# Performance work log

Hardware: AMD Instinct MI355X
Metric: run time of the kernel (lower is better)

Reference implementation:

```python
import jax, jax.numpy as jnp
import numpy as np

B, S, H = 2, 2048, 1024
NUM_HEADS = 16
HEAD_DIM = H // NUM_HEADS  # 64
SCALE = HEAD_DIM ** -0.5


def apply_rope(x, cos, sin):
    # x: [B, nh, S, hd]; cos/sin: [1, 1, S, hd//2]
    x1 = x[..., ::2]
    x2 = x[..., 1::2]
    rotated = jnp.stack([x1 * cos - x2 * sin, x1 * sin + x2 * cos], axis=-1)
    return rotated.reshape(x.shape)


def setup_inputs() -> dict:
    key = jax.random.key(0)
    ks = jax.random.split(key, 7)
    return {
        "x": jax.random.normal(ks[0], (B, S, H), dtype=jnp.float32),
        "cos": jax.random.normal(ks[1], (S, HEAD_DIM // 2), dtype=jnp.float32),
        "sin": jax.random.normal(ks[2], (S, HEAD_DIM // 2), dtype=jnp.float32),
        "wq": jax.random.normal(ks[3], (H, H), dtype=jnp.float32) * (H ** -0.5),
        "wk": jax.random.normal(ks[4], (H, H), dtype=jnp.float32) * (H ** -0.5),
        "wv": jax.random.normal(ks[5], (H, H), dtype=jnp.float32) * (H ** -0.5),
        "wo": jax.random.normal(ks[6], (H, H), dtype=jnp.float32) * (H ** -0.5),
    }


def reference(x, cos, sin, wq, wk, wv, wo):
    b, s, h = x.shape
    nh, hd = NUM_HEADS, HEAD_DIM
    # torch Linear: y = x @ W.T
    q = (x @ wq.T).reshape(b, s, nh, hd).transpose(0, 2, 1, 3)  # [b, nh, s, hd]
    k = (x @ wk.T).reshape(b, s, nh, hd).transpose(0, 2, 1, 3)
    v = (x @ wv.T).reshape(b, s, nh, hd).transpose(0, 2, 1, 3)

    c = cos[None, None]  # [1,1,s,hd//2]
    sn = sin[None, None]
    q = apply_rope(q, c, sn)
    k = apply_rope(k, c, sn)

    scores = jnp.einsum("bhqd,bhkd->bhqk", q, k) * SCALE  # [b, nh, s, s]
    causal_mask = jnp.triu(jnp.ones((s, s), dtype=bool), k=1)
    scores = jnp.where(causal_mask[None, None], -jnp.inf, scores)
    attn = jax.nn.softmax(scores, axis=-1)
    out = jnp.einsum("bhqk,bhkd->bhqd", attn, v)  # [b, nh, s, hd]
    out = out.transpose(0, 2, 1, 3).reshape(b, s, h)
    return out @ wo.T
```

## Files before the change

### kernel.cpp

```cpp
#include <hip/hip_runtime.h>

typedef __attribute__((ext_vector_type(8))) __bf16 bf16x8;
typedef __attribute__((ext_vector_type(4))) float f32x4;
typedef __attribute__((ext_vector_type(4))) unsigned short ushort4v;

__device__ __forceinline__ unsigned short f2bf(float x) {
  union { float f; unsigned u; } v; v.f = x;
  unsigned r = v.u + 0x7fffu + ((v.u >> 16) & 1u);
  return (unsigned short)(r >> 16);
}

#define GLDS16(g, l) __builtin_amdgcn_global_load_lds( \
    (__attribute__((address_space(1))) void*)(g), \
    (__attribute__((address_space(3))) void*)(l), 16, 0, 0)

__global__ void cvt_f32_bf16(const float* __restrict__ src,
                             unsigned short* __restrict__ dst, int n4) {
  int i = blockIdx.x * blockDim.x + threadIdx.x;
  if (i >= n4) return;
  float4 v = reinterpret_cast<const float4*>(src)[i];
  ushort4v o;
  o.x = f2bf(v.x); o.y = f2bf(v.y); o.z = f2bf(v.z); o.w = f2bf(v.w);
  reinterpret_cast<ushort4v*>(dst)[i] = o;
}

template <int MODE>
__global__ __launch_bounds__(256) void gemm_bt(
    const unsigned short* __restrict__ A, const unsigned short* __restrict__ Bw,
    const float* __restrict__ cosT, const float* __restrict__ sinT,
    unsigned short* __restrict__ Qh, unsigned short* __restrict__ Kh,
    unsigned short* __restrict__ Vt, float* __restrict__ outF) {
  __shared__ __align__(16) unsigned char smA[2][8192];
  __shared__ __align__(16) unsigned char smB[2][8192];
  const int t = threadIdx.x;
  const int lane = t & 63, wvi = t >> 6;
  const int wr = wvi >> 1, wc = wvi & 1;
  const int g = lane >> 4, li = lane & 15;
  const int row0 = blockIdx.y * 128, col0 = blockIdx.x * 128;

  const int schunk = (t & 3) ^ ((t >> 2) & 3);
  const size_t arow = (size_t)(row0 + (t >> 2)) * 1024 + schunk * 8;
  const size_t brow = (size_t)(col0 + (t >> 2)) * 1024 + schunk * 8;

  f32x4 acc[4][4];
#pragma unroll
  for (int mi = 0; mi < 4; ++mi)
#pragma unroll
    for (int ni = 0; ni < 4; ++ni) acc[mi][ni] = (f32x4){0.f, 0.f, 0.f, 0.f};

  auto stage = [&](int buf, int k0) {
    GLDS16(A + arow + k0, &smA[buf][t * 16]);
    GLDS16(A + arow + 64 * 1024 + k0, &smA[buf][4096 + t * 16]);
    GLDS16(Bw + brow + k0, &smB[buf][t * 16]);
    GLDS16(Bw + brow + 64 * 1024 + k0, &smB[buf][4096 + t * 16]);
  };

  stage(0, 0);
  for (int kk = 0; kk < 32; ++kk) {
    __syncthreads();
    const int buf = kk & 1;
    if (kk < 31) stage(buf ^ 1, (kk + 1) * 32);
    bf16x8 af[4], bfr[4];
#pragma unroll
    for (int mi = 0; mi < 4; ++mi)
      af[mi] = *reinterpret_cast<const bf16x8*>(
          &smA[buf][((wr * 64 + mi * 16 + li) << 6) + ((g ^ (li & 3)) << 4)]);
#pragma unroll
    for (int ni = 0; ni < 4; ++ni)
      bfr[ni] = *reinterpret_cast<const bf16x8*>(
          &smB[buf][((wc * 64 + ni * 16 + li) << 6) + ((g ^ (li & 3)) << 4)]);
#pragma unroll
    for (int mi = 0; mi < 4; ++mi)
#pragma unroll
      for (int ni = 0; ni < 4; ++ni)
        acc[mi][ni] = __builtin_amdgcn_mfma_f32_16x16x32_bf16(
            af[mi], bfr[ni], acc[mi][ni], 0, 0, 0);
  }

#pragma unroll
  for (int mi = 0; mi < 4; ++mi) {
    const int rowb = row0 + wr * 64 + mi * 16 + g * 4;
#pragma unroll
    for (int ni = 0; ni < 4; ++ni) {
      const int col = col0 + wc * 64 + ni * 16 + li;
#pragma unroll
      for (int r = 0; r < 4; ++r) {
        float v = acc[mi][ni][r];
        const int rr = rowb + r;
        if (MODE == 1) {
          outF[(size_t)rr * 1024 + col] = v;
        } else {
          const int s = rr & 2047, b = rr >> 11;
          const int jj = col & 1023;
          const int h = jj >> 6, d = jj & 63;
          const int bh = b * 16 + h;
          const int typ = col >> 10;
          if (typ == 2) {
            Vt[((size_t)bh * 64 + d) * 2048 + s] = f2bf(v);
          } else {
            const float cs = cosT[s * 32 + (d >> 1)];
            const float sn = sinT[s * 32 + (d >> 1)];
            const float pr = __shfl_xor(v, 1);
            float rv = (d & 1) ? (pr * sn + v * cs) : (v * cs - pr * sn);
            if (typ == 0) rv *= 0.125f;
            unsigned short* dst = (typ == 0) ? Qh : Kh;
            dst[((size_t)bh * 2048 + s) * 64 + d] = f2bf(rv);
          }
        }
      }
    }
  }
}

__global__ __launch_bounds__(256) void attn_fwd(
    const unsigned short* __restrict__ Qh, const unsigned short* __restrict__ Kh,
    const unsigned short* __restrict__ Vt, unsigned short* __restrict__ Ob) {
  __shared__ __align__(16) unsigned char smK[2][8192];
  __shared__ __align__(16) unsigned char smV[2][8192];
  __shared__ __align__(16) unsigned short Plds[4][16][72];

  const int t = threadIdx.x, lane = t & 63, w = t >> 6;
  const int g = lane >> 4, li = lane & 15;
  const int qt = blockIdx.x, bh = blockIdx.y;
  const int q0 = qt * 64;

  bf16x8 qa[2];
  {
    const unsigned short* qrow =
        Qh + ((size_t)bh * 2048 + q0 + w * 16 + li) * 64 + g * 8;
    qa[0] = *reinterpret_cast<const bf16x8*>(qrow);
    qa[1] = *reinterpret_cast<const bf16x8*>(qrow + 32);
  }

  float m_[4], l_[4];
  f32x4 oacc[4];
#pragma unroll
  for (int r = 0; r < 4; ++r) { m_[r] = -1e30f; l_[r] = 0.f; }
#pragma unroll
  for (int dt = 0; dt < 4; ++dt) oacc[dt] = (f32x4){0.f, 0.f, 0.f, 0.f};

  const int ntile = qt + 1;

  auto stage = [&](int buf, int kt) {
    const int kv0 = kt * 64;
#pragma unroll
    for (int i = 0; i < 2; ++i) {
      const int e = i * 256 + t;
      const int row = e >> 3;
      const int sc = (e & 7) ^ (row & 7);
      GLDS16(Kh + ((size_t)bh * 2048 + kv0 + row) * 64 + sc * 8, &smK[buf][e * 16]);
      GLDS16(Vt + ((size_t)bh * 64 + row) * 2048 + kv0 + sc * 8, &smV[buf][e * 16]);
    }
  };

  stage(0, 0);
  for (int kt = 0; kt < ntile; ++kt) {
    __syncthreads();
    const int buf = kt & 1;
    if (kt + 1 < ntile) stage(buf ^ 1, kt + 1);

    f32x4 sacc[4];
#pragma unroll
    for (int ct = 0; ct < 4; ++ct) {
      const int rb = (ct * 16 + li) << 7;
      bf16x8 kb0 = *reinterpret_cast<const bf16x8*>(
          &smK[buf][rb + (((0 * 4 + g) ^ (li & 7)) << 4)]);
      bf16x8 kb1 = *reinterpret_cast<const bf16x8*>(
          &smK[buf][rb + (((1 * 4 + g) ^ (li & 7)) << 4)]);
      f32x4 z = (f32x4){0.f, 0.f, 0.f, 0.f};
      z = __builtin_amdgcn_mfma_f32_16x16x32_bf16(qa[0], kb0, z, 0, 0, 0);
      z = __builtin_amdgcn_mfma_f32_16x16x32_bf16(qa[1], kb1, z, 0, 0, 0);
      sacc[ct] = z;
    }
    if (kt == qt) {
#pragma unroll
      for (int ct = 0; ct < 4; ++ct)
#pragma unroll
        for (int r = 0; r < 4; ++r)
          if (ct * 16 + li > w * 16 + g * 4 + r) sacc[ct][r] = -1e30f;
    }
    float mnew[4], alpha[4], psum[4];
#pragma unroll
    for (int r = 0; r < 4; ++r) {
      float tm = fmaxf(fmaxf(sacc[0][r], sacc[1][r]), fmaxf(sacc[2][r], sacc[3][r]));
      tm = fmaxf(tm, __shfl_xor(tm, 1));
      tm = fmaxf(tm, __shfl_xor(tm, 2));
      tm = fmaxf(tm, __shfl_xor(tm, 4));
      tm = fmaxf(tm, __shfl_xor(tm, 8));
      const float mn = fmaxf(m_[r], tm);
      mnew[r] = mn;
      alpha[r] = __expf(m_[r] - mn);
      m_[r] = mn;
      psum[r] = 0.f;
    }
#pragma unroll
    for (int ct = 0; ct < 4; ++ct)
#pragma unroll
      for (int r = 0; r < 4; ++r) {
        const float p = __expf(sacc[ct][r] - mnew[r]);
        psum[r] += p;
        Plds[w][g * 4 + r][ct * 16 + li] = f2bf(p);
      }
#pragma unroll
    for (int r = 0; r < 4; ++r) {
      float ps = psum[r];
      ps += __shfl_xor(ps, 1);
      ps += __shfl_xor(ps, 2);
      ps += __shfl_xor(ps, 4);
      ps += __shfl_xor(ps, 8);
      l_[r] = l_[r] * alpha[r] + ps;
#pragma unroll
      for (int dt = 0; dt < 4; ++dt) oacc[dt][r] *= alpha[r];
    }
    __builtin_amdgcn_wave_barrier();
    bf16x8 pa0, pa1;
    __builtin_memcpy(&pa0, &Plds[w][li][g * 8], 16);
    __builtin_memcpy(&pa1, &Plds[w][li][32 + g * 8], 16);
#pragma unroll
    for (int dt = 0; dt < 4; ++dt) {
      const int rb = (dt * 16 + li) << 7;
      bf16x8 vb0 = *reinterpret_cast<const bf16x8*>(
          &smV[buf][rb + (((0 * 4 + g) ^ (li & 7)) << 4)]);
      bf16x8 vb1 = *reinterpret_cast<const bf16x8*>(
          &smV[buf][rb + (((1 * 4 + g) ^ (li & 7)) << 4)]);
      oacc[dt] = __builtin_amdgcn_mfma_f32_16x16x32_bf16(pa0, vb0, oacc[dt], 0, 0, 0);
      oacc[dt] = __builtin_amdgcn_mfma_f32_16x16x32_bf16(pa1, vb1, oacc[dt], 0, 0, 0);
    }
  }

  const int b = bh >> 4, h = bh & 15;
#pragma unroll
  for (int r = 0; r < 4; ++r) {
    const float inv = 1.0f / l_[r];
    const int row = q0 + w * 16 + g * 4 + r;
#pragma unroll
    for (int dt = 0; dt < 4; ++dt)
      Ob[((size_t)b * 2048 + row) * 1024 + h * 64 + dt * 16 + li] =
          f2bf(oacc[dt][r] * inv);
  }
}

extern "C" void kernel_launch(void* const* d_in, const int* in_sizes, int n_in,
                              void* d_out, int out_size, void* d_ws, size_t ws_size,
                              hipStream_t stream) {
  const float* x = (const float*)d_in[0];
  const float* cosT = (const float*)d_in[1];
  const float* sinT = (const float*)d_in[2];
  const float* wq = (const float*)d_in[3];
  const float* wk = (const float*)d_in[4];
  const float* wv = (const float*)d_in[5];
  const float* wo = (const float*)d_in[6];
  float* out = (float*)d_out;

  char* ws = (char*)d_ws;
  unsigned short* xb    = (unsigned short*)(ws);
  unsigned short* wqkvb = (unsigned short*)(ws + 8388608);
  unsigned short* wob   = (unsigned short*)(ws + 14680064);
  unsigned short* Qh    = (unsigned short*)(ws + 16777216);
  unsigned short* Kh    = (unsigned short*)(ws + 25165824);
  unsigned short* Vt    = (unsigned short*)(ws + 33554432);
  unsigned short* Ob    = (unsigned short*)(ws + 41943040);

  cvt_f32_bf16<<<4096, 256, 0, stream>>>(x, xb, 1048576);
  cvt_f32_bf16<<<1024, 256, 0, stream>>>(wq, wqkvb, 262144);
  cvt_f32_bf16<<<1024, 256, 0, stream>>>(wk, wqkvb + 1048576, 262144);
  cvt_f32_bf16<<<1024, 256, 0, stream>>>(wv, wqkvb + 2097152, 262144);
  cvt_f32_bf16<<<1024, 256, 0, stream>>>(wo, wob, 262144);

  gemm_bt<0><<<dim3(24, 32), 256, 0, stream>>>(xb, wqkvb, cosT, sinT, Qh, Kh, Vt,
                                               nullptr);
  attn_fwd<<<dim3(32, 32), 256, 0, stream>>>(Qh, Kh, Vt, Ob);
  gemm_bt<1><<<dim3(8, 32), 256, 0, stream>>>(Ob, wob, nullptr, nullptr, nullptr,
                                              nullptr, nullptr, out);
}
```

Measured before the change: 292.7 us.

## Load K/V directly from global into registers and use exp2 softmax

The attention kernel drops the double-buffered LDS staging of K and V. Each wave now loads its K and V MFMA operands straight from global memory into registers. The log2(e) factor is folded into the Q pre-scale so softmax can use the native exp2 instruction, and the grid is reordered so the head index is in blockIdx.x. Occupancy is also hinted via launch bounds. Dropping LDS removes its footprint and the staging copies, but all four waves now re-read the same K/V tiles through the cache and lose the async prefetch overlap.

```diff
diff --git a/kernel.cpp b/kernel.cpp
--- a/kernel.cpp
+++ b/kernel.cpp
@@ -102,7 +102,7 @@
             const float sn = sinT[s * 32 + (d >> 1)];
             const float pr = __shfl_xor(v, 1);
             float rv = (d & 1) ? (pr * sn + v * cs) : (v * cs - pr * sn);
-            if (typ == 0) rv *= 0.125f;
+            if (typ == 0) rv *= 0.18033688011112042f;
             unsigned short* dst = (typ == 0) ? Qh : Kh;
             dst[((size_t)bh * 2048 + s) * 64 + d] = f2bf(rv);
           }
@@ -112,17 +112,18 @@
   }
 }
 
-__global__ __launch_bounds__(256) void attn_fwd(
+__global__ __launch_bounds__(256, 4) void attn_fwd(
     const unsigned short* __restrict__ Qh, const unsigned short* __restrict__ Kh,
     const unsigned short* __restrict__ Vt, unsigned short* __restrict__ Ob) {
-  __shared__ __align__(16) unsigned char smK[2][8192];
-  __shared__ __align__(16) unsigned char smV[2][8192];
   __shared__ __align__(16) unsigned short Plds[4][16][72];
 
   const int t = threadIdx.x, lane = t & 63, w = t >> 6;
   const int g = lane >> 4, li = lane & 15;
-  const int qt = blockIdx.x, bh = blockIdx.y;
+  const int bh = blockIdx.x, qt = blockIdx.y;
   const int q0 = qt * 64;
+
+  const unsigned short* __restrict__ Kbh = Kh + (size_t)bh * 2048 * 64;
+  const unsigned short* __restrict__ Vbh = Vt + (size_t)bh * 64 * 2048;
 
   bf16x8 qa[2];
   {
@@ -139,39 +140,29 @@
 #pragma unroll
   for (int dt = 0; dt < 4; ++dt) oacc[dt] = (f32x4){0.f, 0.f, 0.f, 0.f};
 
-  const int ntile = qt + 1;
-
-  auto stage = [&](int buf, int kt) {
+  for (int kt = 0; kt <= qt; ++kt) {
     const int kv0 = kt * 64;
-#pragma unroll
-    for (int i = 0; i < 2; ++i) {
-      const int e = i * 256 + t;
-      const int row = e >> 3;
-      const int sc = (e & 7) ^ (row & 7);
-      GLDS16(Kh + ((size_t)bh * 2048 + kv0 + row) * 64 + sc * 8, &smK[buf][e * 16]);
-      GLDS16(Vt + ((size_t)bh * 64 + row) * 2048 + kv0 + sc * 8, &smV[buf][e * 16]);
-    }
-  };
-
-  stage(0, 0);
-  for (int kt = 0; kt < ntile; ++kt) {
-    __syncthreads();
-    const int buf = kt & 1;
-    if (kt + 1 < ntile) stage(buf ^ 1, kt + 1);
 
     f32x4 sacc[4];
 #pragma unroll
     for (int ct = 0; ct < 4; ++ct) {
-      const int rb = (ct * 16 + li) << 7;
-      bf16x8 kb0 = *reinterpret_cast<const bf16x8*>(
-          &smK[buf][rb + (((0 * 4 + g) ^ (li & 7)) << 4)]);
-      bf16x8 kb1 = *reinterpret_cast<const bf16x8*>(
-          &smK[buf][rb + (((1 * 4 + g) ^ (li & 7)) << 4)]);
+      const unsigned short* krow = Kbh + (size_t)(kv0 + ct * 16 + li) * 64 + g * 8;
+      bf16x8 kb0 = *reinterpret_cast<const bf16x8*>(krow);
+      bf16x8 kb1 = *reinterpret_cast<const bf16x8*>(krow + 32);
       f32x4 z = (f32x4){0.f, 0.f, 0.f, 0.f};
       z = __builtin_amdgcn_mfma_f32_16x16x32_bf16(qa[0], kb0, z, 0, 0, 0);
       z = __builtin_amdgcn_mfma_f32_16x16x32_bf16(qa[1], kb1, z, 0, 0, 0);
       sacc[ct] = z;
     }
+
+    bf16x8 vb[8];
+#pragma unroll
+    for (int dt = 0; dt < 4; ++dt) {
+      const unsigned short* vrow = Vbh + (size_t)(dt * 16 + li) * 2048 + kv0 + g * 8;
+      vb[2 * dt] = *reinterpret_cast<const bf16x8*>(vrow);
+      vb[2 * dt + 1] = *reinterpret_cast<const bf16x8*>(vrow + 32);
+    }
+
     if (kt == qt) {
 #pragma unroll
       for (int ct = 0; ct < 4; ++ct)
@@ -179,6 +170,7 @@
         for (int r = 0; r < 4; ++r)
           if (ct * 16 + li > w * 16 + g * 4 + r) sacc[ct][r] = -1e30f;
     }
+
     float mnew[4], alpha[4], psum[4];
 #pragma unroll
     for (int r = 0; r < 4; ++r) {
@@ -189,7 +181,7 @@
       tm = fmaxf(tm, __shfl_xor(tm, 8));
       const float mn = fmaxf(m_[r], tm);
       mnew[r] = mn;
-      alpha[r] = __expf(m_[r] - mn);
+      alpha[r] = __builtin_amdgcn_exp2f(m_[r] - mn);
       m_[r] = mn;
       psum[r] = 0.f;
     }
@@ -197,7 +189,7 @@
     for (int ct = 0; ct < 4; ++ct)
 #pragma unroll
       for (int r = 0; r < 4; ++r) {
-        const float p = __expf(sacc[ct][r] - mnew[r]);
+        const float p = __builtin_amdgcn_exp2f(sacc[ct][r] - mnew[r]);
         psum[r] += p;
         Plds[w][g * 4 + r][ct * 16 + li] = f2bf(p);
       }
@@ -216,16 +208,13 @@
     bf16x8 pa0, pa1;
     __builtin_memcpy(&pa0, &Plds[w][li][g * 8], 16);
     __builtin_memcpy(&pa1, &Plds[w][li][32 + g * 8], 16);
+    __builtin_amdgcn_sched_barrier(0);
 #pragma unroll
     for (int dt = 0; dt < 4; ++dt) {
-      const int rb = (dt * 16 + li) << 7;
-      bf16x8 vb0 = *reinterpret_cast<const bf16x8*>(
-          &smV[buf][rb + (((0 * 4 + g) ^ (li & 7)) << 4)]);
-      bf16x8 vb1 = *reinterpret_cast<const bf16x8*>(
-          &smV[buf][rb + (((1 * 4 + g) ^ (li & 7)) << 4)]);
-      oacc[dt] = __builtin_amdgcn_mfma_f32_16x16x32_bf16(pa0, vb0, oacc[dt], 0, 0, 0);
-      oacc[dt] = __builtin_amdgcn_mfma_f32_16x16x32_bf16(pa1, vb1, oacc[dt], 0, 0, 0);
-    }
+      oacc[dt] = __builtin_amdgcn_mfma_f32_16x16x32_bf16(pa0, vb[2 * dt], oacc[dt], 0, 0, 0);
+      oacc[dt] = __builtin_amdgcn_mfma_f32_16x16x32_bf16(pa1, vb[2 * dt + 1], oacc[dt], 0, 0, 0);
+    }
+    __syncthreads();
   }
 
   const int b = bh >> 4, h = bh & 15;
```

Measured after the change: 324.5 us. 1.11x slower.
